# Kernel tuning notes

Measured on AMD Instinct MI355X. Metric: run time of the kernel, lower is better.

The kernel has to match this reference:

```python
import jax, jax.numpy as jnp
import numpy as np

B, C, N, K, H = 8, 32, 4096, 32, 4  # batch, d_model, num_points, knn, heads
D = C // H
LN_EPS = 1e-5
ATT_EPS = 1e-6


def setup_inputs() -> dict:
    key = jax.random.key(0)
    ks = jax.random.split(key, 12)
    s = 0.05
    return {
        "search_feat": jax.random.normal(ks[0], (B, C, N), jnp.float32),
        "search_xyz": jax.random.normal(ks[1], (B, N, 3), jnp.float32),
        # pos MLP: Linear(3,32)+ReLU+Linear(32,32), weights stored [in,out]
        "w_pos1": jax.random.normal(ks[2], (3, 32), jnp.float32) * s,
        "b_pos1": jnp.zeros((32,), jnp.float32),
        "w_pos2": jax.random.normal(ks[3], (32, 32), jnp.float32) * s,
        "b_pos2": jnp.zeros((32,), jnp.float32),
        "w_q": jax.random.normal(ks[4], (C, C), jnp.float32) * s,
        "w_k": jax.random.normal(ks[5], (C, C), jnp.float32) * s,
        "w_v": jax.random.normal(ks[6], (C, C), jnp.float32) * s,
        "w_merge": jax.random.normal(ks[7], (C, C), jnp.float32) * s,
        "ln1_g": jnp.ones((C,), jnp.float32),
        "ln1_b": jnp.zeros((C,), jnp.float32),
        "w_mlp1": jax.random.normal(ks[8], (2 * C, 2 * C), jnp.float32) * s,
        "w_mlp2": jax.random.normal(ks[9], (2 * C, C), jnp.float32) * s,
        "ln2_g": jnp.ones((C,), jnp.float32),
        "ln2_b": jnp.zeros((C,), jnp.float32),
    }


def _layernorm(x, g, b):
    m = jnp.mean(x, axis=-1, keepdims=True)
    v = jnp.mean((x - m) ** 2, axis=-1, keepdims=True)
    return g * (x - m) * jax.lax.rsqrt(v + LN_EPS) + b


def _elu1(x):
    return jax.nn.elu(x) + 1.0


def reference(search_feat, search_xyz, w_pos1, b_pos1, w_pos2, b_pos2,
              w_q, w_k, w_v, w_merge, ln1_g, ln1_b, w_mlp1, w_mlp2,
              ln2_g, ln2_b):
    b, c, n = search_feat.shape
    h, d, k = H, C // H, K

    xt = jnp.transpose(search_feat, (0, 2, 1))  # [B,N,C]
    # knn in feature space: pd = -||xi||^2 + 2 xi.xj - ||xj||^2 (neg sq dist)
    xx = jnp.sum(xt * xt, axis=-1)  # [B,N]
    pd = 2.0 * jnp.einsum('bnc,bmc->bnm', xt, xt) - xx[:, :, None] - xx[:, None, :]
    idx = jax.lax.top_k(pd, k)[1]  # [B,N,K] nearest (incl. self)

    gather = jax.vmap(lambda f, i: f[i])  # per-batch gather
    fea_knn = gather(xt, idx)            # [B,N,K,C]
    xyz_knn = gather(search_xyz, idx)    # [B,N,K,3]

    def pos_mlp(z):
        return jax.nn.relu(z @ w_pos1 + b_pos1) @ w_pos2 + b_pos2

    q_in = xt + pos_mlp(search_xyz)      # [B,N,C]  (query, L=1)
    kv_in = fea_knn + pos_mlp(xyz_knn)   # [B,N,K,C]

    Q = (q_in @ w_q).reshape(b, n, h, d)          # [B,N,H,D]
    Ky = (kv_in @ w_k).reshape(b, n, k, h, d)     # [B,N,K,H,D]
    V = (kv_in @ w_v).reshape(b, n, k, h, d)

    Qf = _elu1(Q)
    Kf = _elu1(Ky)
    Vn = V / k  # v_length = K
    KV = jnp.einsum('bnkhd,bnkhv->bnhdv', Kf, Vn)
    Z = 1.0 / (jnp.einsum('bnhd,bnhd->bnh', Qf, Kf.sum(axis=2)) + ATT_EPS)
    msg = jnp.einsum('bnhd,bnhdv,bnh->bnhv', Qf, KV, Z) * k  # [B,N,H,D]

    msg = msg.reshape(b, n, c) @ w_merge
    msg = _layernorm(msg, ln1_g, ln1_b)
    msg = jnp.concatenate([xt, msg], axis=-1)          # [B,N,2C]
    msg = jax.nn.relu(msg @ w_mlp1) @ w_mlp2           # [B,N,C]
    msg = _layernorm(msg, ln2_g, ln2_b)
    return jnp.transpose(xt + msg, (0, 2, 1))          # [B,C,N]
```

## Files before the change

### kernel.cpp

```cpp
#include <hip/hip_runtime.h>
#include <math.h>

#define BB 8
#define CC 32
#define NN 4096
#define KNN 32
#define NP (BB*NN)

#define OFF_XT  0u
#define OFF_QF  1048576u
#define OFF_KV  2097152u
#define OFF_XX  4194304u
#define OFF_IDX 4227072u
#define OFF_XH  5275648u
#define OFF_XL  5799936u
#define OFF_MSG 5275648u

typedef _Float16 f16x8 __attribute__((ext_vector_type(8)));
typedef float f32x4 __attribute__((ext_vector_type(4)));
#define MFMA16(A,B,C) __builtin_amdgcn_mfma_f32_16x16x32_f16(A,B,C,0,0,0)

__device__ __forceinline__ float elu1(float x) {
    return x > 0.f ? x + 1.f : expf(x);
}

__global__ __launch_bounds__(256) void k_transpose(const float* __restrict__ feat,
                                                   float* __restrict__ xt,
                                                   _Float16* __restrict__ Xh,
                                                   _Float16* __restrict__ Xl,
                                                   float* __restrict__ xx) {
    __shared__ float tile[32][65];
    int b = blockIdx.y;
    int n0 = blockIdx.x * 64;
    int t = threadIdx.x;
    int nn = t & 63, cr = t >> 6;
#pragma unroll
    for (int r = 0; r < 8; ++r) {
        int c = r * 4 + cr;
        tile[c][nn] = feat[((size_t)b * 32 + c) * NN + n0 + nn];
    }
    __syncthreads();
    int c2 = t & 31, nr = t >> 5;
#pragma unroll
    for (int r = 0; r < 8; ++r) {
        int nl = r * 8 + nr;
        size_t gi = ((size_t)b * NN + n0 + nl) * 32 + c2;
        float v = tile[c2][nl];
        xt[gi] = v;
        _Float16 hv = (_Float16)v;
        Xh[gi] = hv;
        Xl[gi] = (_Float16)(v - (float)hv);
    }
    if (t < 64) {
        float s = 0.f;
#pragma unroll
        for (int c = 0; c < 32; ++c) { float u = tile[c][t]; s += u * u; }
        xx[(size_t)b * NN + n0 + t] = s;
    }
}

__global__ __launch_bounds__(256, 2) void k_prep(
        const float* __restrict__ xt, const float* __restrict__ xyz,
        const float* __restrict__ w_pos1, const float* __restrict__ b_pos1,
        const float* __restrict__ w_pos2, const float* __restrict__ b_pos2,
        const float* __restrict__ w_q, const float* __restrict__ w_k,
        const float* __restrict__ w_v,
        float* __restrict__ Qf, float* __restrict__ KV) {
    __shared__ float sW2[1024], sWq[1024], sWk[1024], sWv[1024];
    int t = threadIdx.x;
    for (int i = t; i < 1024; i += 256) {
        sW2[i] = w_pos2[i];
        sWq[i] = w_q[i];
        sWk[i] = w_k[i];
        sWv[i] = w_v[i];
    }
    int lane = t & 31;
    int g = t >> 5;
    float w1c0 = w_pos1[lane], w1c1 = w_pos1[32 + lane], w1c2 = w_pos1[64 + lane];
    float b1c = b_pos1[lane], b2c = b_pos2[lane];
    __syncthreads();
#pragma unroll 1
    for (int p = blockIdx.x * 8 + g; p < NP; p += gridDim.x * 8) {
        asm volatile("" ::: "memory");
        float x0 = xyz[(size_t)p * 3 + 0];
        float x1 = xyz[(size_t)p * 3 + 1];
        float x2 = xyz[(size_t)p * 3 + 2];
        float h = fmaxf(x0 * w1c0 + x1 * w1c1 + x2 * w1c2 + b1c, 0.f);
        float P = b2c;
#pragma unroll 8
        for (int j = 0; j < 32; ++j) P += __shfl(h, j, 32) * sW2[j * 32 + lane];
        float xv = xt[(size_t)p * 32 + lane];
        float qin = xv + P;
        float qa = 0.f, ka = 0.f, va = 0.f;
#pragma unroll 8
        for (int j = 0; j < 32; ++j) {
            float qj = __shfl(qin, j, 32);
            qa += qj * sWq[j * 32 + lane];
            ka += qj * sWk[j * 32 + lane];
            va += qj * sWv[j * 32 + lane];
        }
        Qf[(size_t)p * 32 + lane] = elu1(qa);
        float2 kvv;
        kvv.x = elu1(ka);
        kvv.y = va;
        *(((float2*)(KV + (size_t)p * 64)) + lane) = kvv;
    }
}

__global__ __launch_bounds__(256, 4) void k_knn(
        const _Float16* __restrict__ Xh, const _Float16* __restrict__ Xl,
        const float* __restrict__ xt, const float* __restrict__ xx,
        unsigned* __restrict__ idxg) {
    __shared__ unsigned histU[32 * 128];
    __shared__ unsigned outIdx[32][32];
    __shared__ unsigned tieIdx[32][96];
    __shared__ int sT[32];
    __shared__ unsigned sBase[32];
    __shared__ unsigned outCnt[32], tieCnt[32];
    __shared__ float sM2;
    __shared__ float redbuf[4];

    int bid = blockIdx.x;
    int b = bid & 7;
    int n0 = (bid >> 3) << 5;
    int t = threadIdx.x;
    int lane = t & 63, wv = t >> 6;
    size_t bbase = (size_t)b * NN;

    for (int i = t; i < 4096; i += 256) histU[i] = 0u;
    if (t < 32) { outCnt[t] = 0u; tieCnt[t] = 0u; }

    float lm = 0.f;
    for (int i = t; i < NN; i += 256) lm = fmaxf(lm, xx[bbase + i]);
#pragma unroll
    for (int off = 32; off >= 1; off >>= 1) lm = fmaxf(lm, __shfl_xor(lm, off, 64));
    if (lane == 0) redbuf[wv] = lm;
    __syncthreads();
    if (t == 0) sM2 = fmaxf(fmaxf(redbuf[0], redbuf[1]), fmaxf(redbuf[2], redbuf[3]));
    __syncthreads();
    float M2 = sM2;

    int al = lane & 15;
    int kgrp = lane >> 4;
    int ak = kgrp * 8;
    const _Float16* Xhb = Xh + bbase * 32;
    const _Float16* Xlb = Xl + bbase * 32;
    const float* xxb = xx + bbase;
    f16x8 Ah0 = *(const f16x8*)(Xhb + (size_t)(n0 + al) * 32 + ak);
    f16x8 Al0 = *(const f16x8*)(Xlb + (size_t)(n0 + al) * 32 + ak);
    f16x8 Ah1 = *(const f16x8*)(Xhb + (size_t)(n0 + 16 + al) * 32 + ak);
    f16x8 Al1 = *(const f16x8*)(Xlb + (size_t)(n0 + 16 + al) * 32 + ak);

    const float C511 = 511.96f;
    float sc2[8], scn[8], c0a[8];
    unsigned rowW[8];
#pragma unroll
    for (int r = 0; r < 8; ++r) {
        int rowloc = (r < 4 ? 0 : 16) + kgrp * 4 + (r & 3);
        float xxi = xxb[n0 + rowloc];
        float scale = C511 / (2.f * (xxi + M2));
        sc2[r] = scale + scale;
        scn[r] = -scale;
        c0a[r] = __builtin_fmaf(-xxi, scale, C511);
        rowW[r] = (unsigned)rowloc * 128u;
    }

    unsigned cp0 = (unsigned)(wv * 1024 + al);
    unsigned akB = (unsigned)ak * 2u;
    const char* XhbB = (const char*)Xhb;
    const char* XlbB = (const char*)Xlb;

    {
        f16x8 Bh_c = *(const f16x8*)(XhbB + cp0 * 64u + akB);
        f16x8 Bl_c = *(const f16x8*)(XlbB + cp0 * 64u + akB);
        float xxj_c = xxb[cp0];
#pragma unroll 1
        for (int tt = 0; tt < 64; ++tt) {
            unsigned cpn = cp0 + (unsigned)(((tt + 1) & 63) << 4);
            f16x8 Bh_n = *(const f16x8*)(XhbB + cpn * 64u + akB);
            f16x8 Bl_n = *(const f16x8*)(XlbB + cpn * 64u + akB);
            float xxj_n = xxb[cpn];
            f32x4 z = {0.f, 0.f, 0.f, 0.f};
            f32x4 u0 = MFMA16(Al0, Bl_c, z); u0 = MFMA16(Ah0, Bl_c, u0);
            f32x4 w0 = MFMA16(Al0, Bh_c, z); w0 = MFMA16(Ah0, Bh_c, w0);
            f32x4 u1 = MFMA16(Al1, Bl_c, z); u1 = MFMA16(Ah1, Bl_c, u1);
            f32x4 w1 = MFMA16(Al1, Bh_c, z); w1 = MFMA16(Ah1, Bh_c, w1);
            float bcol[8];
#pragma unroll
            for (int r = 0; r < 8; ++r) bcol[r] = __builtin_fmaf(xxj_c, scn[r], c0a[r]);
#pragma unroll
            for (int r = 0; r < 8; ++r) {
                float a = (r < 4) ? (u0[r] + w0[r]) : (u1[r - 4] + w1[r - 4]);
                float qf = __builtin_fmaf(a, sc2[r], bcol[r]);
                unsigned q = (unsigned)fmaxf(qf, 0.f);
                q = q > 511u ? 511u : q;
                atomicAdd(&histU[rowW[r] + (q >> 2)], 1u);
            }
            Bh_c = Bh_n; Bl_c = Bl_n; xxj_c = xxj_n;
        }
    }
    __syncthreads();

#pragma unroll 1
    for (int rr = 0; rr < 8; ++rr) {
        int row = wv * 8 + rr;
        const unsigned* Hr = histU + row * 128;
        unsigned cl = Hr[2 * lane], ch = Hr[2 * lane + 1];
        unsigned ss = cl + ch;
        unsigned acc = ss;
#pragma unroll
        for (int off = 1; off < 64; off <<= 1) {
            unsigned vv = __shfl_down(acc, off, 64);
            if (lane + off < 64) acc += vv;
        }
        unsigned run = acc - ss;
        int Tl = -1; unsigned bl = 0;
        if (run < 32u && run + ch >= 32u) { Tl = 2 * lane + 1; bl = run; }
        run += ch;
        if (Tl < 0 && run < 32u && run + cl >= 32u) { Tl = 2 * lane; bl = run; }
        unsigned long long bal = __ballot(Tl >= 0);
        int src = __ffsll(bal) - 1;
        int Tv = __shfl(Tl, src, 64);
        unsigned bv = (unsigned)__shfl((int)bl, src, 64);
        if (lane == 0) { sT[row] = Tv; sBase[row] = bv; }
    }
    __syncthreads();

    float Tin[8], Tlo[8];
#pragma unroll
    for (int r = 0; r < 8; ++r) {
        int T = sT[rowW[r] >> 7];
        Tin[r] = (float)(4 * T + 4);
        Tlo[r] = (T == 0) ? -3.0e38f : (float)(4 * T);
    }

    {
        f16x8 Bh_c = *(const f16x8*)(XhbB + cp0 * 64u + akB);
        f16x8 Bl_c = *(const f16x8*)(XlbB + cp0 * 64u + akB);
        float xxj_c = xxb[cp0];
#pragma unroll 1
        for (int tt = 0; tt < 64; ++tt) {
            unsigned cp = cp0 + (unsigned)(tt << 4);
            unsigned cpn = cp0 + (unsigned)(((tt + 1) & 63) << 4);
            f16x8 Bh_n = *(const f16x8*)(XhbB + cpn * 64u + akB);
            f16x8 Bl_n = *(const f16x8*)(XlbB + cpn * 64u + akB);
            float xxj_n = xxb[cpn];
            f32x4 z = {0.f, 0.f, 0.f, 0.f};
            f32x4 u0 = MFMA16(Al0, Bl_c, z); u0 = MFMA16(Ah0, Bl_c, u0);
            f32x4 w0 = MFMA16(Al0, Bh_c, z); w0 = MFMA16(Ah0, Bh_c, w0);
            f32x4 u1 = MFMA16(Al1, Bl_c, z); u1 = MFMA16(Ah1, Bl_c, u1);
            f32x4 w1 = MFMA16(Al1, Bh_c, z); w1 = MFMA16(Ah1, Bh_c, w1);
            float bcol[8];
#pragma unroll
            for (int r = 0; r < 8; ++r) bcol[r] = __builtin_fmaf(xxj_c, scn[r], c0a[r]);
#pragma unroll
            for (int r = 0; r < 8; ++r) {
                float a = (r < 4) ? (u0[r] + w0[r]) : (u1[r - 4] + w1[r - 4]);
                float qf = __builtin_fmaf(a, sc2[r], bcol[r]);
                if (qf >= Tlo[r]) {
                    unsigned row = rowW[r] >> 7;
                    if (qf >= Tin[r]) {
                        unsigned pos = atomicAdd(&outCnt[row], 1u);
                        outIdx[row][pos] = cp;
                    } else {
                        unsigned tp = atomicAdd(&tieCnt[row], 1u);
                        if (tp < 96u) tieIdx[row][tp] = cp;
                    }
                }
            }
            Bh_c = Bh_n; Bl_c = Bl_n; xxj_c = xxj_n;
        }
    }
    __syncthreads();

#pragma unroll 1
    for (int rr = 0; rr < 8; ++rr) {
        int row = wv * 8 + rr;
        int gr = n0 + row;
        unsigned bA = sBase[row];
        int need = 32 - (int)bA;
        if (need <= 0) continue;
        int nt = (int)tieCnt[row]; if (nt > 96) nt = 96;
        const float* xr = xt + (bbase + gr) * 32;
        float xxi_r = xxb[gr];
        float v0 = -INFINITY, v1 = -INFINITY;
        int i0 = 0x7fffffff, i1 = 0x7fffffff;
        bool a0v = lane < nt, a1v = lane + 64 < nt;
        if (a0v) {
            int c = (int)tieIdx[row][lane];
            const float* xc = xt + (bbase + c) * 32;
            float dot = 0.f;
#pragma unroll
            for (int ch = 0; ch < 32; ch += 4) {
                float4 rv = *(const float4*)(xr + ch);
                float4 cv = *(const float4*)(xc + ch);
                dot = __builtin_fmaf(rv.x, cv.x, dot);
                dot = __builtin_fmaf(rv.y, cv.y, dot);
                dot = __builtin_fmaf(rv.z, cv.z, dot);
                dot = __builtin_fmaf(rv.w, cv.w, dot);
            }
            v0 = 2.f * dot - xxi_r - xxb[c];
            i0 = c;
        }
        if (a1v) {
            int c = (int)tieIdx[row][lane + 64];
            const float* xc = xt + (bbase + c) * 32;
            float dot = 0.f;
#pragma unroll
            for (int ch = 0; ch < 32; ch += 4) {
                float4 rv = *(const float4*)(xr + ch);
                float4 cv = *(const float4*)(xc + ch);
                dot = __builtin_fmaf(rv.x, cv.x, dot);
                dot = __builtin_fmaf(rv.y, cv.y, dot);
                dot = __builtin_fmaf(rv.z, cv.z, dot);
                dot = __builtin_fmaf(rv.w, cv.w, dot);
            }
            v1 = 2.f * dot - xxi_r - xxb[c];
            i1 = c;
        }
        for (int it = 0; it < need; ++it) {
            float bvv = -INFINITY; int bj2 = 0x7fffffff;
            if (a0v && (v0 > bvv || (v0 == bvv && i0 < bj2))) { bvv = v0; bj2 = i0; }
            if (a1v && (v1 > bvv || (v1 == bvv && i1 < bj2))) { bvv = v1; bj2 = i1; }
#pragma unroll
            for (int off = 1; off < 64; off <<= 1) {
                float ov = __shfl_xor(bvv, off, 64);
                int oj = __shfl_xor(bj2, off, 64);
                if (ov > bvv || (ov == bvv && oj < bj2)) { bvv = ov; bj2 = oj; }
            }
            if (a0v && i0 == bj2) a0v = false;
            if (a1v && i1 == bj2) a1v = false;
            if (lane == 0) outIdx[row][bA + it] = (unsigned)bj2;
        }
    }
    __syncthreads();

    for (int i = t; i < 1024; i += 256)
        idxg[(bbase + n0 + (i >> 5)) * 32 + (i & 31)] = outIdx[i >> 5][i & 31];
}

__global__ __launch_bounds__(256) void k_attn(
        const float* __restrict__ Qf, const float* __restrict__ KV,
        const unsigned* __restrict__ idxg, float* __restrict__ msg) {
    int t = threadIdx.x;
    int wv = t >> 6, lane = t & 63;
    int l32 = lane & 31;
    int p = blockIdx.x * 8 + wv * 2 + (lane >> 5);
    int b = p >> 12;
    size_t bbase = (size_t)b * NN;
    const char* KVb = (const char*)(KV + bbase * 64);
    float q = Qf[(size_t)p * 32 + l32];
    int jv = (int)idxg[(size_t)p * 32 + l32];
    unsigned laneoff = (unsigned)l32 * 8u;
    float zacc = 0.f, macc = 0.f;
#pragma unroll 8
    for (int k = 0; k < 32; ++k) {
        int j = __shfl(jv, k, 32);
        unsigned off = ((unsigned)j << 8) + laneoff;
        float2 kv = *(const float2*)(KVb + off);
        float s = q * kv.x;
        s += __shfl_xor(s, 1, 8);
        s += __shfl_xor(s, 2, 8);
        s += __shfl_xor(s, 4, 8);
        zacc += s;
        macc = __builtin_fmaf(s, kv.y, macc);
    }
    float Z = 1.f / (zacc + 1e-6f);
    msg[(size_t)p * 32 + l32] = macc * Z;
}

__global__ __launch_bounds__(256, 2) void k_post(
        const float* __restrict__ msg, const float* __restrict__ xt,
        const float* __restrict__ w_merge,
        const float* __restrict__ ln1_g, const float* __restrict__ ln1_b,
        const float* __restrict__ w_mlp1, const float* __restrict__ w_mlp2,
        const float* __restrict__ ln2_g, const float* __restrict__ ln2_b,
        float* __restrict__ out) {
    __shared__ _Float16 wmT[2][32][32];
    __shared__ _Float16 w1T[2][64][64];
    __shared__ _Float16 w2T[2][32][64];
    __shared__ _Float16 sPh[4][16][40], sPl[4][16][40];
    __shared__ _Float16 sHh[4][16][72], sHl[4][16][72];
    int t = threadIdx.x;
    for (int i = t; i < 1024; i += 256) {
        float v = w_merge[i]; int in = i >> 5, o = i & 31;
        _Float16 h = (_Float16)v;
        wmT[0][o][in] = h; wmT[1][o][in] = (_Float16)(v - (float)h);
    }
    for (int i = t; i < 4096; i += 256) {
        float v = w_mlp1[i]; int in = i >> 6, o = i & 63;
        _Float16 h = (_Float16)v;
        w1T[0][o][in] = h; w1T[1][o][in] = (_Float16)(v - (float)h);
    }
    for (int i = t; i < 2048; i += 256) {
        float v = w_mlp2[i]; int in = i >> 5, o = i & 31;
        _Float16 h = (_Float16)v;
        w2T[0][o][in] = h; w2T[1][o][in] = (_Float16)(v - (float)h);
    }
    int wv = t >> 6, lane = t & 63;
    int row = lane & 15, kg = lane >> 4;
    int p0 = blockIdx.x * 64 + wv * 16;
    int b = p0 >> 12;
    float g1a = ln1_g[row], b1a = ln1_b[row], g1b = ln1_g[row + 16], b1b = ln1_b[row + 16];
    float g2a = ln2_g[row], b2a = ln2_b[row], g2b = ln2_g[row + 16], b2b = ln2_b[row + 16];
    __syncthreads();

    f32x4 z4 = {0.f, 0.f, 0.f, 0.f};
    f16x8 Amh, Aml;
    {
        const float* mr = msg + (size_t)(p0 + row) * 32 + kg * 8;
#pragma unroll
        for (int j = 0; j < 8; ++j) {
            float v = mr[j];
            _Float16 h = (_Float16)v;
            Amh[j] = h; Aml[j] = (_Float16)(v - (float)h);
        }
    }
    f32x4 accM[2];
#pragma unroll
    for (int n = 0; n < 2; ++n) {
        f16x8 Bh = *(const f16x8*)&wmT[0][n * 16 + row][kg * 8];
        f16x8 Bl = *(const f16x8*)&wmT[1][n * 16 + row][kg * 8];
        f32x4 a = z4;
        a = MFMA16(Aml, Bl, a); a = MFMA16(Amh, Bl, a);
        a = MFMA16(Aml, Bh, a); a = MFMA16(Amh, Bh, a);
        accM[n] = a;
    }
#pragma unroll
    for (int r = 0; r < 4; ++r) {
        float s0 = accM[0][r], s1 = accM[1][r];
        float sm = s0 + s1;
        sm += __shfl_xor(sm, 1, 64); sm += __shfl_xor(sm, 2, 64);
        sm += __shfl_xor(sm, 4, 64); sm += __shfl_xor(sm, 8, 64);
        float mean = sm * (1.f / 32.f);
        float d0 = s0 - mean, d1 = s1 - mean;
        float vv = d0 * d0 + d1 * d1;
        vv += __shfl_xor(vv, 1, 64); vv += __shfl_xor(vv, 2, 64);
        vv += __shfl_xor(vv, 4, 64); vv += __shfl_xor(vv, 8, 64);
        float rst = rsqrtf(vv * (1.f / 32.f) + 1e-5f);
        float m0 = g1a * d0 * rst + b1a;
        float m1 = g1b * d1 * rst + b1b;
        int pl = kg * 4 + r;
        _Float16 h0 = (_Float16)m0;
        sPh[wv][pl][row] = h0; sPl[wv][pl][row] = (_Float16)(m0 - (float)h0);
        _Float16 h1 = (_Float16)m1;
        sPh[wv][pl][row + 16] = h1; sPl[wv][pl][row + 16] = (_Float16)(m1 - (float)h1);
    }
    __syncthreads();
    f16x8 Axh, Axl;
    {
        const float* xr = xt + (size_t)(p0 + row) * 32 + kg * 8;
#pragma unroll
        for (int j = 0; j < 8; ++j) {
            float v = xr[j];
            _Float16 h = (_Float16)v;
            Axh[j] = h; Axl[j] = (_Float16)(v - (float)h);
        }
    }
    f16x8 Aph = *(const f16x8*)&sPh[wv][row][kg * 8];
    f16x8 Apl = *(const f16x8*)&sPl[wv][row][kg * 8];
    f32x4 accH[4];
#pragma unroll
    for (int n = 0; n < 4; ++n) {
        f16x8 B0h = *(const f16x8*)&w1T[0][n * 16 + row][kg * 8];
        f16x8 B0l = *(const f16x8*)&w1T[1][n * 16 + row][kg * 8];
        f16x8 B1h = *(const f16x8*)&w1T[0][n * 16 + row][32 + kg * 8];
        f16x8 B1l = *(const f16x8*)&w1T[1][n * 16 + row][32 + kg * 8];
        f32x4 a = z4;
        a = MFMA16(Axl, B0l, a); a = MFMA16(Axh, B0l, a);
        a = MFMA16(Axl, B0h, a); a = MFMA16(Axh, B0h, a);
        a = MFMA16(Apl, B1l, a); a = MFMA16(Aph, B1l, a);
        a = MFMA16(Apl, B1h, a); a = MFMA16(Aph, B1h, a);
        accH[n] = a;
    }
#pragma unroll
    for (int n = 0; n < 4; ++n) {
#pragma unroll
        for (int r = 0; r < 4; ++r) {
            float hv = fmaxf(accH[n][r], 0.f);
            int pl = kg * 4 + r;
            _Float16 hh = (_Float16)hv;
            sHh[wv][pl][n * 16 + row] = hh;
            sHl[wv][pl][n * 16 + row] = (_Float16)(hv - (float)hh);
        }
    }
    __syncthreads();
    f16x8 Hh0 = *(const f16x8*)&sHh[wv][row][kg * 8];
    f16x8 Hl0 = *(const f16x8*)&sHl[wv][row][kg * 8];
    f16x8 Hh1 = *(const f16x8*)&sHh[wv][row][32 + kg * 8];
    f16x8 Hl1 = *(const f16x8*)&sHl[wv][row][32 + kg * 8];
    f32x4 accO[2];
#pragma unroll
    for (int n = 0; n < 2; ++n) {
        f16x8 B0h = *(const f16x8*)&w2T[0][n * 16 + row][kg * 8];
        f16x8 B0l = *(const f16x8*)&w2T[1][n * 16 + row][kg * 8];
        f16x8 B1h = *(const f16x8*)&w2T[0][n * 16 + row][32 + kg * 8];
        f16x8 B1l = *(const f16x8*)&w2T[1][n * 16 + row][32 + kg * 8];
        f32x4 a = z4;
        a = MFMA16(Hl0, B0l, a); a = MFMA16(Hh0, B0l, a);
        a = MFMA16(Hl0, B0h, a); a = MFMA16(Hh0, B0h, a);
        a = MFMA16(Hl1, B1l, a); a = MFMA16(Hh1, B1l, a);
        a = MFMA16(Hl1, B1h, a); a = MFMA16(Hh1, B1h, a);
        accO[n] = a;
    }
#pragma unroll
    for (int r = 0; r < 4; ++r) {
        float s0 = accO[0][r], s1 = accO[1][r];
        float sm = s0 + s1;
        sm += __shfl_xor(sm, 1, 64); sm += __shfl_xor(sm, 2, 64);
        sm += __shfl_xor(sm, 4, 64); sm += __shfl_xor(sm, 8, 64);
        float mean = sm * (1.f / 32.f);
        float d0 = s0 - mean, d1 = s1 - mean;
        float vv = d0 * d0 + d1 * d1;
        vv += __shfl_xor(vv, 1, 64); vv += __shfl_xor(vv, 2, 64);
        vv += __shfl_xor(vv, 4, 64); vv += __shfl_xor(vv, 8, 64);
        float rst = rsqrtf(vv * (1.f / 32.f) + 1e-5f);
        float o0 = g2a * d0 * rst + b2a;
        float o1 = g2b * d1 * rst + b2b;
        int pt = p0 + kg * 4 + r;
        int nb = pt & 4095;
        float xv0 = xt[(size_t)pt * 32 + row];
        float xv1 = xt[(size_t)pt * 32 + row + 16];
        out[((size_t)b * 32 + row) * 4096 + nb] = xv0 + o0;
        out[((size_t)b * 32 + row + 16) * 4096 + nb] = xv1 + o1;
    }
}

extern "C" void kernel_launch(void* const* d_in, const int* in_sizes, int n_in,
                              void* d_out, int out_size, void* d_ws, size_t ws_size,
                              hipStream_t stream) {
    const float* feat   = (const float*)d_in[0];
    const float* xyz    = (const float*)d_in[1];
    const float* w_pos1 = (const float*)d_in[2];
    const float* b_pos1 = (const float*)d_in[3];
    const float* w_pos2 = (const float*)d_in[4];
    const float* b_pos2 = (const float*)d_in[5];
    const float* w_q    = (const float*)d_in[6];
    const float* w_k    = (const float*)d_in[7];
    const float* w_v    = (const float*)d_in[8];
    const float* w_mg   = (const float*)d_in[9];
    const float* ln1_g  = (const float*)d_in[10];
    const float* ln1_b  = (const float*)d_in[11];
    const float* w_mlp1 = (const float*)d_in[12];
    const float* w_mlp2 = (const float*)d_in[13];
    const float* ln2_g  = (const float*)d_in[14];
    const float* ln2_b  = (const float*)d_in[15];
    float* ws = (float*)d_ws;
    float* xt = ws + OFF_XT;
    float* Qf = ws + OFF_QF;
    float* KVp = ws + OFF_KV;
    float* xx = ws + OFF_XX;
    unsigned* idxg = (unsigned*)(ws + OFF_IDX);
    _Float16* Xh = (_Float16*)(ws + OFF_XH);
    _Float16* Xl = (_Float16*)(ws + OFF_XL);
    float* msg = ws + OFF_MSG;
    float* out = (float*)d_out;

    k_transpose<<<dim3(64, 8), 256, 0, stream>>>(feat, xt, Xh, Xl, xx);
    k_prep<<<1024, 256, 0, stream>>>(xt, xyz, w_pos1, b_pos1, w_pos2, b_pos2,
                                     w_q, w_k, w_v, Qf, KVp);
    k_knn<<<1024, 256, 0, stream>>>(Xh, Xl, xt, xx, idxg);
    k_attn<<<4096, 256, 0, stream>>>(Qf, KVp, idxg, msg);
    k_post<<<512, 256, 0, stream>>>(msg, xt, w_mg, ln1_g, ln1_b,
                                    w_mlp1, w_mlp2, ln2_g, ln2_b, out);
}
```

Before: 247.3 us.

## Prefilter KNN histogram with sample-based floor and pad histogram rows

The KNN kernel now first bins a sample of 128 candidates per row into a 128-bin histogram to derive a lower floor for the top-32 threshold. In the main pass it only does LDS atomic increments for candidates above that floor. Bins are unit-width instead of 4-wide, and each histogram row is padded to 132 entries to reduce LDS bank conflicts. The goal is to cut the LDS atomic traffic in the histogram pass, at the cost of a small extra sampling pass and a conditional branch per candidate.

```diff
diff --git a/kernel.cpp b/kernel.cpp
--- a/kernel.cpp
+++ b/kernel.cpp
@@ -111,11 +111,12 @@
         const _Float16* __restrict__ Xh, const _Float16* __restrict__ Xl,
         const float* __restrict__ xt, const float* __restrict__ xx,
         unsigned* __restrict__ idxg) {
-    __shared__ unsigned histU[32 * 128];
+    __shared__ unsigned histU[32 * 132];
     __shared__ unsigned outIdx[32][32];
     __shared__ unsigned tieIdx[32][96];
     __shared__ int sT[32];
     __shared__ unsigned sBase[32];
+    __shared__ float sFloor[32];
     __shared__ unsigned outCnt[32], tieCnt[32];
     __shared__ float sM2;
     __shared__ float redbuf[4];
@@ -127,7 +128,7 @@
     int lane = t & 63, wv = t >> 6;
     size_t bbase = (size_t)b * NN;
 
-    for (int i = t; i < 4096; i += 256) histU[i] = 0u;
+    for (int i = t; i < 32 * 132; i += 256) histU[i] = 0u;
     if (t < 32) { outCnt[t] = 0u; tieCnt[t] = 0u; }
 
     float lm = 0.f;
@@ -151,18 +152,20 @@
     f16x8 Ah1 = *(const f16x8*)(Xhb + (size_t)(n0 + 16 + al) * 32 + ak);
     f16x8 Al1 = *(const f16x8*)(Xlb + (size_t)(n0 + 16 + al) * 32 + ak);
 
-    const float C511 = 511.96f;
+    const float C127 = 127.99f;
     float sc2[8], scn[8], c0a[8];
     unsigned rowW[8];
+    int rowloc8[8];
 #pragma unroll
     for (int r = 0; r < 8; ++r) {
         int rowloc = (r < 4 ? 0 : 16) + kgrp * 4 + (r & 3);
         float xxi = xxb[n0 + rowloc];
-        float scale = C511 / (2.f * (xxi + M2));
+        float scale = C127 / (2.f * (xxi + M2));
         sc2[r] = scale + scale;
         scn[r] = -scale;
-        c0a[r] = __builtin_fmaf(-xxi, scale, C511);
-        rowW[r] = (unsigned)rowloc * 128u;
+        c0a[r] = __builtin_fmaf(-xxi, scale, C127);
+        rowW[r] = (unsigned)rowloc * 132u;
+        rowloc8[r] = rowloc;
     }
 
     unsigned cp0 = (unsigned)(wv * 1024 + al);
@@ -170,13 +173,65 @@
     const char* XhbB = (const char*)Xhb;
     const char* XlbB = (const char*)Xlb;
 
+#pragma unroll 1
+    for (int tt = 0; tt < 8; ++tt) {
+        unsigned cp = cp0 + (unsigned)(tt << 4);
+        f16x8 Bh = *(const f16x8*)(XhbB + cp * 64u + akB);
+        f16x8 Bl = *(const f16x8*)(XlbB + cp * 64u + akB);
+        float xxj = xxb[cp];
+        f32x4 z = {0.f, 0.f, 0.f, 0.f};
+        f32x4 u0 = MFMA16(Al0, Bl, z); u0 = MFMA16(Ah0, Bl, u0);
+        f32x4 w0 = MFMA16(Al0, Bh, z); w0 = MFMA16(Ah0, Bh, w0);
+        f32x4 u1 = MFMA16(Al1, Bl, z); u1 = MFMA16(Ah1, Bl, u1);
+        f32x4 w1 = MFMA16(Al1, Bh, z); w1 = MFMA16(Ah1, Bh, w1);
+#pragma unroll
+        for (int r = 0; r < 8; ++r) {
+            float a = (r < 4) ? (u0[r] + w0[r]) : (u1[r - 4] + w1[r - 4]);
+            float bcol = __builtin_fmaf(xxj, scn[r], c0a[r]);
+            float qf = __builtin_fmaf(a, sc2[r], bcol);
+            float qc = __builtin_amdgcn_fmed3f(qf, 0.f, C127);
+            atomicAdd(&histU[rowW[r] + (unsigned)qc], 1u);
+        }
+    }
+    __syncthreads();
+
+#pragma unroll 1
+    for (int rr = 0; rr < 8; ++rr) {
+        int row = wv * 8 + rr;
+        const unsigned* Hr = histU + row * 132;
+        unsigned cl = Hr[2 * lane], ch = Hr[2 * lane + 1];
+        unsigned ss = cl + ch;
+        unsigned acc = ss;
+#pragma unroll
+        for (int off = 1; off < 64; off <<= 1) {
+            unsigned vv = __shfl_down(acc, off, 64);
+            if (lane + off < 64) acc += vv;
+        }
+        unsigned run = acc - ss;
+        int Tl = -1;
+        if (run < 32u && run + ch >= 32u) Tl = 2 * lane + 1;
+        run += ch;
+        if (Tl < 0 && run < 32u && run + cl >= 32u) Tl = 2 * lane;
+        unsigned long long bal = __ballot(Tl >= 0);
+        int src = __ffsll(bal) - 1;
+        int Tv = __shfl(Tl, src, 64);
+        if (lane == 0) sFloor[row] = (Tv <= 0) ? -3.0e38f : (float)Tv;
+    }
+    __syncthreads();
+
+    float fb1[8];
+#pragma unroll
+    for (int r = 0; r < 8; ++r) fb1[r] = sFloor[rowloc8[r]];
+
     {
-        f16x8 Bh_c = *(const f16x8*)(XhbB + cp0 * 64u + akB);
-        f16x8 Bl_c = *(const f16x8*)(XlbB + cp0 * 64u + akB);
-        float xxj_c = xxb[cp0];
+        unsigned cpc = cp0 + (8u << 4);
+        f16x8 Bh_c = *(const f16x8*)(XhbB + cpc * 64u + akB);
+        f16x8 Bl_c = *(const f16x8*)(XlbB + cpc * 64u + akB);
+        float xxj_c = xxb[cpc];
 #pragma unroll 1
-        for (int tt = 0; tt < 64; ++tt) {
-            unsigned cpn = cp0 + (unsigned)(((tt + 1) & 63) << 4);
+        for (int tt = 8; tt < 64; ++tt) {
+            int tn = (tt + 1 < 64) ? (tt + 1) : 8;
+            unsigned cpn = cp0 + (unsigned)(tn << 4);
             f16x8 Bh_n = *(const f16x8*)(XhbB + cpn * 64u + akB);
             f16x8 Bl_n = *(const f16x8*)(XlbB + cpn * 64u + akB);
             float xxj_n = xxb[cpn];
@@ -192,9 +247,10 @@
             for (int r = 0; r < 8; ++r) {
                 float a = (r < 4) ? (u0[r] + w0[r]) : (u1[r - 4] + w1[r - 4]);
                 float qf = __builtin_fmaf(a, sc2[r], bcol[r]);
-                unsigned q = (unsigned)fmaxf(qf, 0.f);
-                q = q > 511u ? 511u : q;
-                atomicAdd(&histU[rowW[r] + (q >> 2)], 1u);
+                if (qf >= fb1[r]) {
+                    float qc = __builtin_amdgcn_fmed3f(qf, 0.f, C127);
+                    atomicAdd(&histU[rowW[r] + (unsigned)qc], 1u);
+                }
             }
             Bh_c = Bh_n; Bl_c = Bl_n; xxj_c = xxj_n;
         }
@@ -204,7 +260,7 @@
 #pragma unroll 1
     for (int rr = 0; rr < 8; ++rr) {
         int row = wv * 8 + rr;
-        const unsigned* Hr = histU + row * 128;
+        const unsigned* Hr = histU + row * 132;
         unsigned cl = Hr[2 * lane], ch = Hr[2 * lane + 1];
         unsigned ss = cl + ch;
         unsigned acc = ss;
@@ -229,9 +285,9 @@
     float Tin[8], Tlo[8];
 #pragma unroll
     for (int r = 0; r < 8; ++r) {
-        int T = sT[rowW[r] >> 7];
-        Tin[r] = (float)(4 * T + 4);
-        Tlo[r] = (T == 0) ? -3.0e38f : (float)(4 * T);
+        int T = sT[rowloc8[r]];
+        Tin[r] = (float)(T + 1);
+        Tlo[r] = (T == 0) ? -3.0e38f : (float)T;
     }
 
     {
@@ -258,7 +314,7 @@
                 float a = (r < 4) ? (u0[r] + w0[r]) : (u1[r - 4] + w1[r - 4]);
                 float qf = __builtin_fmaf(a, sc2[r], bcol[r]);
                 if (qf >= Tlo[r]) {
-                    unsigned row = rowW[r] >> 7;
+                    unsigned row = rowW[r] / 132u;
                     if (qf >= Tin[r]) {
                         unsigned pos = atomicAdd(&outCnt[row], 1u);
                         outIdx[row][pos] = cp;
```

Result: no change. 242.8 us (-1.8%).

## Switch kNN distance tiles to 32x32 MFMA with row-independent histogram bucketing

Applied to the files above, without the earlier changes.

The kNN kernel now computes distances with 32x32x16 f16 MFMAs instead of 16x16x32. It drops the low*low split-precision product, using 6 MFMAs per tile instead of 8. Quantization uses a single per-batch scale with 128 direct buckets, histogram rows are padded to 132 entries against bank conflicts, the tie buffer is enlarged, and occupancy hints drop to 2. The attention kernel's block-to-point mapping now interleaves batches across blocks. The coarser global bucketing risks larger tie sets for rows with small norms, and dropping the low*low term slightly reduces distance precision.

```diff
diff --git a/kernel.cpp b/kernel.cpp
--- a/kernel.cpp
+++ b/kernel.cpp
@@ -18,7 +18,9 @@
 
 typedef _Float16 f16x8 __attribute__((ext_vector_type(8)));
 typedef float f32x4 __attribute__((ext_vector_type(4)));
+typedef float f32x16 __attribute__((ext_vector_type(16)));
 #define MFMA16(A,B,C) __builtin_amdgcn_mfma_f32_16x16x32_f16(A,B,C,0,0,0)
+#define MFMA32(A,B,C) __builtin_amdgcn_mfma_f32_32x32x16_f16(A,B,C,0,0,0)
 
 __device__ __forceinline__ float elu1(float x) {
     return x > 0.f ? x + 1.f : expf(x);
@@ -107,13 +109,13 @@
     }
 }
 
-__global__ __launch_bounds__(256, 4) void k_knn(
+__global__ __launch_bounds__(256, 2) void k_knn(
         const _Float16* __restrict__ Xh, const _Float16* __restrict__ Xl,
         const float* __restrict__ xt, const float* __restrict__ xx,
         unsigned* __restrict__ idxg) {
-    __shared__ unsigned histU[32 * 128];
+    __shared__ unsigned histU[32 * 132];
     __shared__ unsigned outIdx[32][32];
-    __shared__ unsigned tieIdx[32][96];
+    __shared__ unsigned tieIdx[32][128];
     __shared__ int sT[32];
     __shared__ unsigned sBase[32];
     __shared__ unsigned outCnt[32], tieCnt[32];
@@ -127,7 +129,7 @@
     int lane = t & 63, wv = t >> 6;
     size_t bbase = (size_t)b * NN;
 
-    for (int i = t; i < 4096; i += 256) histU[i] = 0u;
+    for (int i = t; i < 32 * 132; i += 256) histU[i] = 0u;
     if (t < 32) { outCnt[t] = 0u; tieCnt[t] = 0u; }
 
     float lm = 0.f;
@@ -138,65 +140,62 @@
     __syncthreads();
     if (t == 0) sM2 = fmaxf(fmaxf(redbuf[0], redbuf[1]), fmaxf(redbuf[2], redbuf[3]));
     __syncthreads();
-    float M2 = sM2;
-
-    int al = lane & 15;
-    int kgrp = lane >> 4;
-    int ak = kgrp * 8;
+    float M = fmaxf(sM2, 1e-20f);
+
+    const float C127 = 127.99f;
+    float s = C127 / (4.f * M);
+    float s2 = s + s;
+    float sneg = -s;
+    float o = 3.f * s * M;
+
+    int cl31 = lane & 31;
+    int hi = lane >> 5;
+    int hi4 = hi << 2;
     const _Float16* Xhb = Xh + bbase * 32;
     const _Float16* Xlb = Xl + bbase * 32;
     const float* xxb = xx + bbase;
-    f16x8 Ah0 = *(const f16x8*)(Xhb + (size_t)(n0 + al) * 32 + ak);
-    f16x8 Al0 = *(const f16x8*)(Xlb + (size_t)(n0 + al) * 32 + ak);
-    f16x8 Ah1 = *(const f16x8*)(Xhb + (size_t)(n0 + 16 + al) * 32 + ak);
-    f16x8 Al1 = *(const f16x8*)(Xlb + (size_t)(n0 + 16 + al) * 32 + ak);
-
-    const float C511 = 511.96f;
-    float sc2[8], scn[8], c0a[8];
-    unsigned rowW[8];
-#pragma unroll
-    for (int r = 0; r < 8; ++r) {
-        int rowloc = (r < 4 ? 0 : 16) + kgrp * 4 + (r & 3);
-        float xxi = xxb[n0 + rowloc];
-        float scale = C511 / (2.f * (xxi + M2));
-        sc2[r] = scale + scale;
-        scn[r] = -scale;
-        c0a[r] = __builtin_fmaf(-xxi, scale, C511);
-        rowW[r] = (unsigned)rowloc * 128u;
-    }
-
-    unsigned cp0 = (unsigned)(wv * 1024 + al);
-    unsigned akB = (unsigned)ak * 2u;
+
+    const _Float16* ArH = Xhb + (size_t)(n0 + cl31) * 32;
+    const _Float16* ArL = Xlb + (size_t)(n0 + cl31) * 32;
+    f16x8 AhA = *(const f16x8*)(ArH + hi * 8);
+    f16x8 AhB = *(const f16x8*)(ArH + 16 + hi * 8);
+    f16x8 AlA = *(const f16x8*)(ArL + hi * 8);
+    f16x8 AlB = *(const f16x8*)(ArL + 16 + hi * 8);
+
+    unsigned colbase = (unsigned)(wv * 1024);
+    unsigned hiB = (unsigned)hi * 16u;
     const char* XhbB = (const char*)Xhb;
     const char* XlbB = (const char*)Xlb;
+    unsigned hi528 = (unsigned)hi * 528u;
 
     {
-        f16x8 Bh_c = *(const f16x8*)(XhbB + cp0 * 64u + akB);
-        f16x8 Bl_c = *(const f16x8*)(XlbB + cp0 * 64u + akB);
-        float xxj_c = xxb[cp0];
+        unsigned cpc = colbase + cl31;
+        f16x8 BhA_c = *(const f16x8*)(XhbB + cpc * 64u + hiB);
+        f16x8 BhB_c = *(const f16x8*)(XhbB + cpc * 64u + hiB + 32u);
+        f16x8 BlA_c = *(const f16x8*)(XlbB + cpc * 64u + hiB);
+        f16x8 BlB_c = *(const f16x8*)(XlbB + cpc * 64u + hiB + 32u);
+        float xxj_c = xxb[cpc];
 #pragma unroll 1
-        for (int tt = 0; tt < 64; ++tt) {
-            unsigned cpn = cp0 + (unsigned)(((tt + 1) & 63) << 4);
-            f16x8 Bh_n = *(const f16x8*)(XhbB + cpn * 64u + akB);
-            f16x8 Bl_n = *(const f16x8*)(XlbB + cpn * 64u + akB);
+        for (int tt = 0; tt < 32; ++tt) {
+            unsigned cpn = colbase + (unsigned)(((tt + 1) & 31) << 5) + cl31;
+            f16x8 BhA_n = *(const f16x8*)(XhbB + cpn * 64u + hiB);
+            f16x8 BhB_n = *(const f16x8*)(XhbB + cpn * 64u + hiB + 32u);
+            f16x8 BlA_n = *(const f16x8*)(XlbB + cpn * 64u + hiB);
+            f16x8 BlB_n = *(const f16x8*)(XlbB + cpn * 64u + hiB + 32u);
             float xxj_n = xxb[cpn];
-            f32x4 z = {0.f, 0.f, 0.f, 0.f};
-            f32x4 u0 = MFMA16(Al0, Bl_c, z); u0 = MFMA16(Ah0, Bl_c, u0);
-            f32x4 w0 = MFMA16(Al0, Bh_c, z); w0 = MFMA16(Ah0, Bh_c, w0);
-            f32x4 u1 = MFMA16(Al1, Bl_c, z); u1 = MFMA16(Ah1, Bl_c, u1);
-            f32x4 w1 = MFMA16(Al1, Bh_c, z); w1 = MFMA16(Ah1, Bh_c, w1);
-            float bcol[8];
-#pragma unroll
-            for (int r = 0; r < 8; ++r) bcol[r] = __builtin_fmaf(xxj_c, scn[r], c0a[r]);
-#pragma unroll
-            for (int r = 0; r < 8; ++r) {
-                float a = (r < 4) ? (u0[r] + w0[r]) : (u1[r - 4] + w1[r - 4]);
-                float qf = __builtin_fmaf(a, sc2[r], bcol[r]);
-                unsigned q = (unsigned)fmaxf(qf, 0.f);
-                q = q > 511u ? 511u : q;
-                atomicAdd(&histU[rowW[r] + (q >> 2)], 1u);
+            f32x16 acc = {0.f};
+            acc = MFMA32(AhA, BlA_c, acc); acc = MFMA32(AhB, BlB_c, acc);
+            acc = MFMA32(AlA, BhA_c, acc); acc = MFMA32(AlB, BhB_c, acc);
+            acc = MFMA32(AhA, BhA_c, acc); acc = MFMA32(AhB, BhB_c, acc);
+            float e = __builtin_fmaf(sneg, xxj_c, o);
+#pragma unroll
+            for (int r = 0; r < 16; ++r) {
+                float qv = __builtin_fmaf(acc[r], s2, e);
+                float qc = fminf(qv, C127);
+                unsigned bkt = (unsigned)qc;
+                atomicAdd(&histU[(unsigned)(((r & 3) + 8 * (r >> 2)) * 132) + hi528 + bkt], 1u);
             }
-            Bh_c = Bh_n; Bl_c = Bl_n; xxj_c = xxj_n;
+            BhA_c = BhA_n; BhB_c = BhB_n; BlA_c = BlA_n; BlB_c = BlB_n; xxj_c = xxj_n;
         }
     }
     __syncthreads();
@@ -204,7 +203,7 @@
 #pragma unroll 1
     for (int rr = 0; rr < 8; ++rr) {
         int row = wv * 8 + rr;
-        const unsigned* Hr = histU + row * 128;
+        const unsigned* Hr = histU + row * 132;
         unsigned cl = Hr[2 * lane], ch = Hr[2 * lane + 1];
         unsigned ss = cl + ch;
         unsigned acc = ss;
@@ -226,49 +225,51 @@
     }
     __syncthreads();
 
-    float Tin[8], Tlo[8];
-#pragma unroll
-    for (int r = 0; r < 8; ++r) {
-        int T = sT[rowW[r] >> 7];
-        Tin[r] = (float)(4 * T + 4);
-        Tlo[r] = (T == 0) ? -3.0e38f : (float)(4 * T);
+    float Tlo16[16], Tin16[16];
+#pragma unroll
+    for (int r = 0; r < 16; ++r) {
+        int rl = (r & 3) + 8 * (r >> 2) + hi4;
+        int T = sT[rl];
+        Tin16[r] = (float)(T + 1);
+        Tlo16[r] = (T == 0) ? -3.0e38f : (float)T;
     }
 
     {
-        f16x8 Bh_c = *(const f16x8*)(XhbB + cp0 * 64u + akB);
-        f16x8 Bl_c = *(const f16x8*)(XlbB + cp0 * 64u + akB);
-        float xxj_c = xxb[cp0];
+        unsigned cpc = colbase + cl31;
+        f16x8 BhA_c = *(const f16x8*)(XhbB + cpc * 64u + hiB);
+        f16x8 BhB_c = *(const f16x8*)(XhbB + cpc * 64u + hiB + 32u);
+        f16x8 BlA_c = *(const f16x8*)(XlbB + cpc * 64u + hiB);
+        f16x8 BlB_c = *(const f16x8*)(XlbB + cpc * 64u + hiB + 32u);
+        float xxj_c = xxb[cpc];
 #pragma unroll 1
-        for (int tt = 0; tt < 64; ++tt) {
-            unsigned cp = cp0 + (unsigned)(tt << 4);
-            unsigned cpn = cp0 + (unsigned)(((tt + 1) & 63) << 4);
-            f16x8 Bh_n = *(const f16x8*)(XhbB + cpn * 64u + akB);
-            f16x8 Bl_n = *(const f16x8*)(XlbB + cpn * 64u + akB);
+        for (int tt = 0; tt < 32; ++tt) {
+            unsigned cp = colbase + (unsigned)(tt << 5) + cl31;
+            unsigned cpn = colbase + (unsigned)(((tt + 1) & 31) << 5) + cl31;
+            f16x8 BhA_n = *(const f16x8*)(XhbB + cpn * 64u + hiB);
+            f16x8 BhB_n = *(const f16x8*)(XhbB + cpn * 64u + hiB + 32u);
+            f16x8 BlA_n = *(const f16x8*)(XlbB + cpn * 64u + hiB);
+            f16x8 BlB_n = *(const f16x8*)(XlbB + cpn * 64u + hiB + 32u);
             float xxj_n = xxb[cpn];
-            f32x4 z = {0.f, 0.f, 0.f, 0.f};
-            f32x4 u0 = MFMA16(Al0, Bl_c, z); u0 = MFMA16(Ah0, Bl_c, u0);
-            f32x4 w0 = MFMA16(Al0, Bh_c, z); w0 = MFMA16(Ah0, Bh_c, w0);
-            f32x4 u1 = MFMA16(Al1, Bl_c, z); u1 = MFMA16(Ah1, Bl_c, u1);
-            f32x4 w1 = MFMA16(Al1, Bh_c, z); w1 = MFMA16(Ah1, Bh_c, w1);
-            float bcol[8];
-#pragma unroll
-            for (int r = 0; r < 8; ++r) bcol[r] = __builtin_fmaf(xxj_c, scn[r], c0a[r]);
-#pragma unroll
-            for (int r = 0; r < 8; ++r) {
-                float a = (r < 4) ? (u0[r] + w0[r]) : (u1[r - 4] + w1[r - 4]);
-                float qf = __builtin_fmaf(a, sc2[r], bcol[r]);
-                if (qf >= Tlo[r]) {
-                    unsigned row = rowW[r] >> 7;
-                    if (qf >= Tin[r]) {
-                        unsigned pos = atomicAdd(&outCnt[row], 1u);
-                        outIdx[row][pos] = cp;
+            f32x16 acc = {0.f};
+            acc = MFMA32(AhA, BlA_c, acc); acc = MFMA32(AhB, BlB_c, acc);
+            acc = MFMA32(AlA, BhA_c, acc); acc = MFMA32(AlB, BhB_c, acc);
+            acc = MFMA32(AhA, BhA_c, acc); acc = MFMA32(AhB, BhB_c, acc);
+            float e = __builtin_fmaf(sneg, xxj_c, o);
+#pragma unroll
+            for (int r = 0; r < 16; ++r) {
+                float qv = __builtin_fmaf(acc[r], s2, e);
+                if (qv >= Tlo16[r]) {
+                    unsigned rl = (unsigned)((r & 3) + 8 * (r >> 2) + hi4);
+                    if (qv >= Tin16[r]) {
+                        unsigned pos = atomicAdd(&outCnt[rl], 1u);
+                        outIdx[rl][pos] = cp;
                     } else {
-                        unsigned tp = atomicAdd(&tieCnt[row], 1u);
-                        if (tp < 96u) tieIdx[row][tp] = cp;
+                        unsigned tp = atomicAdd(&tieCnt[rl], 1u);
+                        if (tp < 128u) tieIdx[rl][tp] = cp;
                     }
                 }
             }
-            Bh_c = Bh_n; Bl_c = Bl_n; xxj_c = xxj_n;
+            BhA_c = BhA_n; BhB_c = BhB_n; BlA_c = BlA_n; BlB_c = BlB_n; xxj_c = xxj_n;
         }
     }
     __syncthreads();
@@ -280,7 +281,7 @@
         unsigned bA = sBase[row];
         int need = 32 - (int)bA;
         if (need <= 0) continue;
-        int nt = (int)tieCnt[row]; if (nt > 96) nt = 96;
+        int nt = (int)tieCnt[row]; if (nt > 128) nt = 128;
         const float* xr = xt + (bbase + gr) * 32;
         float xxi_r = xxb[gr];
         float v0 = -INFINITY, v1 = -INFINITY;
@@ -345,8 +346,9 @@
     int t = threadIdx.x;
     int wv = t >> 6, lane = t & 63;
     int l32 = lane & 31;
-    int p = blockIdx.x * 8 + wv * 2 + (lane >> 5);
-    int b = p >> 12;
+    int bid = blockIdx.x;
+    int b = bid & 7;
+    int p = b * NN + (bid >> 3) * 8 + wv * 2 + (lane >> 5);
     size_t bbase = (size_t)b * NN;
     const char* KVb = (const char*)(KV + bbase * 64);
     float q = Qf[(size_t)p * 32 + l32];
```

Result: slower. 271.1 us (+9.6%).
